# Kernel tuning notes

Measured on AMD Instinct MI355X. Metric: run time of the kernel, lower is better.

## Reference

```python
import jax, jax.numpy as jnp
import numpy as np

B, S, H = 2, 2048, 2048
NH, KVH, HD = 16, 4, 128
R = 16
LORA_SCALE = 32.0 / 16.0  # lora_alpha / lora_r
ATTN_SCALE = HD ** -0.5
NEG = -1e9


def setup_inputs() -> dict:
    key = jax.random.key(0)
    ks = jax.random.split(key, 16)
    q_dim, kv_dim = NH * HD, KVH * HD
    # RoPE tables
    inv_freq = 1.0 / (10000.0 ** (jnp.arange(0, HD, 2, dtype=jnp.float32) / HD))
    ang = jnp.arange(S, dtype=jnp.float32)[:, None] * inv_freq[None, :]  # [S, HD/2]
    emb = jnp.concatenate([ang, ang], axis=-1)  # [S, HD]
    cos = jnp.broadcast_to(jnp.cos(emb)[None], (B, S, HD))
    sin = jnp.broadcast_to(jnp.sin(emb)[None], (B, S, HD))
    # additive causal mask [B,1,S,S]
    causal = jnp.triu(jnp.full((S, S), NEG, dtype=jnp.float32), k=1)
    attention_mask = jnp.broadcast_to(causal[None, None], (B, 1, S, S))
    return {
        'hidden_states': jax.random.normal(ks[0], (B, S, H), jnp.float32),
        'cos': cos,
        'sin': sin,
        'attention_mask': attention_mask,
        'q_w': jax.random.normal(ks[1], (q_dim, H), jnp.float32) * 0.02,
        'k_w': jax.random.normal(ks[2], (kv_dim, H), jnp.float32) * 0.02,
        'v_w': jax.random.normal(ks[3], (kv_dim, H), jnp.float32) * 0.02,
        'q_b': jax.random.normal(ks[4], (q_dim,), jnp.float32) * 0.02,
        'k_b': jax.random.normal(ks[5], (kv_dim,), jnp.float32) * 0.02,
        'v_b': jax.random.normal(ks[6], (kv_dim,), jnp.float32) * 0.02,
        'q_A': jax.random.normal(ks[7], (H, R), jnp.float32) * (1.0 / np.sqrt(H)),
        'q_B': jax.random.normal(ks[8], (R, q_dim), jnp.float32) * 0.02,
        'k_A': jax.random.normal(ks[9], (H, R), jnp.float32) * (1.0 / np.sqrt(H)),
        'k_B': jax.random.normal(ks[10], (R, kv_dim), jnp.float32) * 0.02,
        'v_A': jax.random.normal(ks[11], (H, R), jnp.float32) * (1.0 / np.sqrt(H)),
        'v_B': jax.random.normal(ks[12], (R, kv_dim), jnp.float32) * 0.02,
        'o_w': jax.random.normal(ks[13], (H, H), jnp.float32) * 0.02,
    }


def _rotate_half(x):
    x1, x2 = x[..., : HD // 2], x[..., HD // 2:]
    return jnp.concatenate([-x2, x1], axis=-1)


def reference(hidden_states, cos, sin, attention_mask,
              q_w, k_w, v_w, q_b, k_b, v_b,
              q_A, q_B, k_A, k_B, v_A, v_B, o_w):
    x = hidden_states  # dropout p=0 (eval)
    # fused base + LoRA projections
    q = x @ q_w.T + q_b + LORA_SCALE * ((x @ q_A) @ q_B)  # [B,S,NH*HD]
    k = x @ k_w.T + k_b + LORA_SCALE * ((x @ k_A) @ k_B)  # [B,S,KVH*HD]
    v = x @ v_w.T + v_b + LORA_SCALE * ((x @ v_A) @ v_B)
    q = q.reshape(B, S, NH, HD).transpose(0, 2, 1, 3)   # [B,NH,S,HD]
    k = k.reshape(B, S, KVH, HD).transpose(0, 2, 1, 3)  # [B,KVH,S,HD]
    v = v.reshape(B, S, KVH, HD).transpose(0, 2, 1, 3)
    # RoPE
    c = cos[:, None]  # [B,1,S,HD]
    s = sin[:, None]
    q = q * c + _rotate_half(q) * s
    k = k * c + _rotate_half(k) * s
    # GQA: repeat kv heads
    n_rep = NH // KVH
    k = jnp.repeat(k, n_rep, axis=1)  # [B,NH,S,HD]
    v = jnp.repeat(v, n_rep, axis=1)
    scores = jnp.einsum('bhqd,bhkd->bhqk', q, k) * ATTN_SCALE
    scores = scores + attention_mask
    attn = jax.nn.softmax(scores.astype(jnp.float32), axis=-1).astype(q.dtype)
    out = jnp.einsum('bhqk,bhkd->bhqd', attn, v)
    out = out.transpose(0, 2, 1, 3).reshape(B, S, NH * HD)  # [B,S,H]
    return out @ o_w.T
```

## Files before the change

### kernel.cpp

```cpp
#include <hip/hip_runtime.h>

constexpr int cB   = 2;
constexpr int cS   = 2048;
constexpr int cH   = 2048;
constexpr int cNH  = 16;
constexpr int cKVH = 4;
constexpr int cHD  = 128;
constexpr int cQD  = 2048;
constexpr int cKVD = 512;
constexpr int cNQKV = 3072;
constexpr int cNTOK = 4096;
#define ATTN_SCALE 0.08838834764831845f
#define QSCALE 0.12751589549581288f

typedef __bf16 bf16;
typedef __attribute__((ext_vector_type(8))) __bf16 bf16x8;
typedef __attribute__((ext_vector_type(4))) __bf16 bf16x4;
typedef __attribute__((ext_vector_type(4))) float  f32x4;

__device__ __forceinline__ void async_load16(const bf16* g, bf16* l) {
    __builtin_amdgcn_global_load_lds(
        (const __attribute__((address_space(1))) void*)g,
        (__attribute__((address_space(3))) void*)l, 16, 0, 0);
}

__global__ void conv_f32_bf16(const float* __restrict__ in, bf16* __restrict__ out) {
    int i = (blockIdx.x * 256 + threadIdx.x) * 4;
    f32x4 v = *(const f32x4*)(in + i);
    bf16x4 o;
    o[0] = (bf16)v[0]; o[1] = (bf16)v[1]; o[2] = (bf16)v[2]; o[3] = (bf16)v[3];
    *(bf16x4*)(out + i) = o;
}

__global__ __launch_bounds__(256) void prep_w2(
        const float* __restrict__ qw, const float* __restrict__ kw, const float* __restrict__ vw,
        const float* __restrict__ qA, const float* __restrict__ qB,
        const float* __restrict__ kA, const float* __restrict__ kB,
        const float* __restrict__ vA, const float* __restrict__ vB,
        const float* __restrict__ qb, const float* __restrict__ kbias, const float* __restrict__ vb,
        bf16* __restrict__ Wc, float* __restrict__ biasc) {
    const int wave = threadIdx.x >> 6, lane = threadIdx.x & 63;
    const int n = blockIdx.y * 4 + wave;
    const int k0 = blockIdx.x * 512 + lane * 8;
    const float* W; const float* Am; const float* Bm; const float* bias; int nn, nd;
    if (n < cQD)             { W = qw; Am = qA; Bm = qB; bias = qb;    nn = n;               nd = cQD; }
    else if (n < cQD + cKVD) { W = kw; Am = kA; Bm = kB; bias = kbias; nn = n - cQD;         nd = cKVD; }
    else                     { W = vw; Am = vA; Bm = vB; bias = vb;    nn = n - cQD - cKVD;  nd = cKVD; }
    if (blockIdx.x == 0 && lane == 0) biasc[n] = bias[nn];
    float bm[16];
    #pragma unroll
    for (int r = 0; r < 16; ++r) bm[r] = Bm[r * nd + nn];
    const float* wrow = W + (size_t)nn * cH + k0;
    f32x4 w0 = *(const f32x4*)(wrow);
    f32x4 w1 = *(const f32x4*)(wrow + 4);
    bf16x8 o;
    #pragma unroll
    for (int j = 0; j < 8; ++j) {
        const f32x4* am = (const f32x4*)(Am + (size_t)(k0 + j) * 16);
        f32x4 a0 = am[0], a1 = am[1], a2 = am[2], a3 = am[3];
        float acc = 0.f;
        #pragma unroll
        for (int c = 0; c < 4; ++c) acc += a0[c] * bm[c] + a1[c] * bm[4 + c]
                                         + a2[c] * bm[8 + c] + a3[c] * bm[12 + c];
        const float wv = (j < 4) ? w0[j] : w1[j - 4];
        o[j] = (bf16)(wv + 2.0f * acc);
    }
    *(bf16x8*)&Wc[(size_t)n * cH + k0] = o;
}

__global__ __launch_bounds__(256) void gemm_qkv(const bf16* __restrict__ A, const bf16* __restrict__ Bw,
                                                const float* __restrict__ bias,
                                                const float* __restrict__ cosb, const float* __restrict__ sinb,
                                                bf16* __restrict__ Qr, bf16* __restrict__ Kr,
                                                bf16* __restrict__ Vt) {
    __shared__ bf16 Al[128 * 64];
    __shared__ bf16 Bl[128 * 64];
    const int tid = threadIdx.x;
    const int wave = tid >> 6, lane = tid & 63;
    const int quad = lane >> 4, l16 = lane & 15;
    const int wr = wave >> 1, wc = wave & 1;
    const long bm = (long)blockIdx.y * 128, bn = (long)blockIdx.x * 128;
    const int K = cH;

    f32x4 acc[4][4];
    #pragma unroll
    for (int i = 0; i < 4; ++i)
        #pragma unroll
        for (int c = 0; c < 4; ++c) acc[i][c] = f32x4{0.f, 0.f, 0.f, 0.f};

    int ago[4], slo[4];
    #pragma unroll
    for (int i2 = 0; i2 < 4; ++i2) {
        const int si = i2 * 256 + tid;
        const int row = si >> 3, c8 = si & 7;
        const int csw = c8 ^ (row & 7);
        ago[i2] = row * K + csw * 8;
        slo[i2] = si * 8;
    }
    const size_t bmK = (size_t)bm * K, bnK = (size_t)bn * K;
    const int sw = l16 & 7;

    for (int k0 = 0; k0 < K; k0 += 64) {
        __syncthreads();
        #pragma unroll
        for (int i2 = 0; i2 < 4; ++i2) async_load16(A  + bmK + k0 + ago[i2], Al + slo[i2]);
        #pragma unroll
        for (int i2 = 0; i2 < 4; ++i2) async_load16(Bw + bnK + k0 + ago[i2], Bl + slo[i2]);
        __syncthreads();
        #pragma unroll
        for (int ks = 0; ks < 2; ++ks) {
            const int g = ks * 4 + quad;
            const int cofs = (g ^ sw) * 8;
            bf16x8 af[4], bfr[4];
            #pragma unroll
            for (int i = 0; i < 4; ++i)
                af[i] = *(const bf16x8*)&Al[(wr * 64 + i * 16 + l16) * 64 + cofs];
            #pragma unroll
            for (int c = 0; c < 4; ++c) {
                const int nrow = wc * 32 + (c & 1) * 16 + (c >> 1) * 64 + l16;
                bfr[c] = *(const bf16x8*)&Bl[nrow * 64 + cofs];
            }
            #pragma unroll
            for (int i = 0; i < 4; ++i)
                #pragma unroll
                for (int c = 0; c < 4; ++c)
                    acc[i][c] = __builtin_amdgcn_mfma_f32_16x16x32_bf16(af[i], bfr[c], acc[i][c], 0, 0, 0);
        }
    }

    #pragma unroll
    for (int c = 0; c < 4; ++c) {
        const int nloc = wc * 32 + (c & 1) * 16 + (c >> 1) * 64 + l16;
        const float bv = bias[bn + nloc];
        #pragma unroll
        for (int i = 0; i < 4; ++i)
            #pragma unroll
            for (int r = 0; r < 4; ++r) acc[i][c][r] += bv;
    }

    const int head = (int)(bn >> 7);
    if (head < cNH + cKVH) {
        const bool isQ = head < cNH;
        #pragma unroll
        for (int cl = 0; cl < 2; ++cl) {
            const int d = wc * 32 + cl * 16 + l16;
            #pragma unroll
            for (int i = 0; i < 4; ++i)
                #pragma unroll
                for (int r = 0; r < 4; ++r) {
                    const long t = bm + wr * 64 + i * 16 + quad * 4 + r;
                    const float cv = cosb[t * cHD + d];
                    const float sv = sinb[t * cHD + d];
                    const float v1 = acc[i][cl][r], v2 = acc[i][cl + 2][r];
                    float o1 = v1 * cv - v2 * sv;
                    float o2 = v2 * cv + v1 * sv;
                    if (isQ) { o1 *= QSCALE; o2 *= QSCALE; }
                    const int b = (int)(t >> 11), s = (int)(t & 2047);
                    bf16* dst = isQ
                        ? Qr + ((size_t)(b * cNH + head) * cS + s) * cHD
                        : Kr + ((size_t)(b * cKVH + (head - cNH)) * cS + s) * cHD;
                    dst[d]      = (bf16)o1;
                    dst[d + 64] = (bf16)o2;
                }
        }
    } else {
        const int kv = head - cNH - cKVH;
        const int b = (int)(bm >> 11);
        const int sbase = (int)(bm & 2047);
        #pragma unroll
        for (int c = 0; c < 4; ++c) {
            const int d = wc * 32 + (c & 1) * 16 + (c >> 1) * 64 + l16;
            #pragma unroll
            for (int i = 0; i < 4; ++i) {
                const int s0 = sbase + wr * 64 + i * 16 + quad * 4;
                bf16x4 o4;
                #pragma unroll
                for (int r = 0; r < 4; ++r) o4[r] = (bf16)acc[i][c][r];
                *(bf16x4*)&Vt[((size_t)((b * cKVH + kv) * cHD) + d) * cS + s0] = o4;
            }
        }
    }
}

__global__ __launch_bounds__(256) void gemm_bt_f32(const bf16* __restrict__ A, const bf16* __restrict__ Bw,
                                                   float* __restrict__ Cp, int M, int N, int K) {
    __shared__ bf16 Al[128 * 64];
    __shared__ bf16 Bl[128 * 64];
    const int tid = threadIdx.x;
    const int wave = tid >> 6, lane = tid & 63;
    const int quad = lane >> 4, l16 = lane & 15;
    const int wr = wave >> 1, wc = wave & 1;
    const long bm = (long)blockIdx.y * 128, bn = (long)blockIdx.x * 128;

    f32x4 acc[4][4];
    #pragma unroll
    for (int i = 0; i < 4; ++i)
        #pragma unroll
        for (int c = 0; c < 4; ++c) acc[i][c] = f32x4{0.f, 0.f, 0.f, 0.f};

    int ago[4], slo[4];
    #pragma unroll
    for (int i2 = 0; i2 < 4; ++i2) {
        const int si = i2 * 256 + tid;
        const int row = si >> 3, c8 = si & 7;
        const int csw = c8 ^ (row & 7);
        ago[i2] = row * K + csw * 8;
        slo[i2] = si * 8;
    }
    const size_t bmK = (size_t)bm * K, bnK = (size_t)bn * K;
    const int sw = l16 & 7;

    for (int k0 = 0; k0 < K; k0 += 64) {
        __syncthreads();
        #pragma unroll
        for (int i2 = 0; i2 < 4; ++i2) async_load16(A  + bmK + k0 + ago[i2], Al + slo[i2]);
        #pragma unroll
        for (int i2 = 0; i2 < 4; ++i2) async_load16(Bw + bnK + k0 + ago[i2], Bl + slo[i2]);
        __syncthreads();
        #pragma unroll
        for (int ks = 0; ks < 2; ++ks) {
            const int cofs = ((ks * 4 + quad) ^ sw) * 8;
            bf16x8 af[4], bfr[4];
            #pragma unroll
            for (int i = 0; i < 4; ++i)
                af[i] = *(const bf16x8*)&Al[(wr * 64 + i * 16 + l16) * 64 + cofs];
            #pragma unroll
            for (int c = 0; c < 4; ++c)
                bfr[c] = *(const bf16x8*)&Bl[(wc * 64 + c * 16 + l16) * 64 + cofs];
            #pragma unroll
            for (int i = 0; i < 4; ++i)
                #pragma unroll
                for (int c = 0; c < 4; ++c)
                    acc[i][c] = __builtin_amdgcn_mfma_f32_16x16x32_bf16(af[i], bfr[c], acc[i][c], 0, 0, 0);
        }
    }

    #pragma unroll
    for (int i = 0; i < 4; ++i)
        #pragma unroll
        for (int c = 0; c < 4; ++c) {
            const long m0 = bm + wr * 64 + i * 16 + quad * 4;
            const long n  = bn + wc * 64 + c * 16 + l16;
            #pragma unroll
            for (int r = 0; r < 4; ++r)
                Cp[(m0 + r) * N + n] = acc[i][c][r];
        }
}

__global__ __launch_bounds__(256, 2) void flash4(const bf16* __restrict__ Q, const bf16* __restrict__ K,
                                                 const bf16* __restrict__ Vt, bf16* __restrict__ Ob) {
    __shared__ bf16 kb[8192];
    __shared__ bf16 vb[8192];
    __shared__ bf16 pb[4096];
    const int tid = threadIdx.x;
    const int wave = tid >> 6, lane = tid & 63;
    const int quad = lane >> 4, l16 = lane & 15;
    const int pi = blockIdx.x;
    const int h = blockIdx.y, b = blockIdx.z;

    const bf16* Qh = Q  + (size_t)(b * cNH + h) * cS * cHD;
    const bf16* Kg = K  + (size_t)(b * cKVH + (h >> 2)) * cS * cHD;
    const bf16* Vg = Vt + (size_t)(b * cKVH + (h >> 2)) * cHD * cS;

    int kgo[4], vgo[4], slo[4];
    #pragma unroll
    for (int i2 = 0; i2 < 4; ++i2) {
        const int si = i2 * 256 + tid;
        const int krow = si >> 4, kcsw = si & 15;
        const int kc = (kcsw & 8) | ((kcsw & 7) ^ (krow & 7));
        kgo[i2] = krow * cHD + kc * 8;
        const int vrow = si >> 3, vcsw = si & 7;
        const int vc = vcsw ^ (vrow & 7);
        vgo[i2] = vrow * cS + vc * 8;
        slo[i2] = si * 8;
    }

    #pragma unroll
    for (int t2 = 0; t2 < 2; ++t2) {
        const int qt = t2 == 0 ? (31 - pi) : pi;

        const bf16* Qg = Qh + (size_t)qt * 64 * cHD;
        bf16x8 qf[4];
        #pragma unroll
        for (int ks = 0; ks < 4; ++ks)
            qf[ks] = *(const bf16x8*)(Qg + (size_t)(wave * 16 + l16) * cHD + ks * 32 + quad * 8);

        f32x4 oac[8];
        #pragma unroll
        for (int dt = 0; dt < 8; ++dt) oac[dt] = f32x4{0.f, 0.f, 0.f, 0.f};
        float m_ = -3.0e38f, l_ = 0.f;

        const int nkt = qt + 1;
        for (int kt = 0; kt < nkt; ++kt) {
            __syncthreads();
            const bf16* Kt  = Kg + (size_t)kt * 64 * cHD;
            const bf16* Vtt = Vg + kt * 64;
            #pragma unroll
            for (int i2 = 0; i2 < 4; ++i2) async_load16(Kt + kgo[i2], kb + slo[i2]);
            #pragma unroll
            for (int i2 = 0; i2 < 4; ++i2) async_load16(Vtt + vgo[i2], vb + slo[i2]);
            __syncthreads();

            f32x4 st[4];
            #pragma unroll
            for (int mt = 0; mt < 4; ++mt) {
                bf16x8 kf[4];
                #pragma unroll
                for (int ks = 0; ks < 4; ++ks) {
                    const int c = ks * 4 + quad;
                    const int csw = (c & 8) | ((c & 7) ^ (l16 & 7));
                    kf[ks] = *(const bf16x8*)&kb[(mt * 16 + l16) * 128 + csw * 8];
                }
                f32x4 a = f32x4{0.f, 0.f, 0.f, 0.f};
                #pragma unroll
                for (int ks = 0; ks < 4; ++ks)
                    a = __builtin_amdgcn_mfma_f32_16x16x32_bf16(kf[ks], qf[ks], a, 0, 0, 0);
                st[mt] = a;
            }

            const int qpos = qt * 64 + wave * 16 + l16;
            float tmax = -3.0e38f;
            if ((kt * 64 + 63) > (qt * 64 + wave * 16)) {
                #pragma unroll
                for (int mt = 0; mt < 4; ++mt)
                    #pragma unroll
                    for (int r = 0; r < 4; ++r) {
                        const int kpos = kt * 64 + mt * 16 + quad * 4 + r;
                        if (kpos > qpos) st[mt][r] = -3.0e38f;
                        tmax = fmaxf(tmax, st[mt][r]);
                    }
            } else {
                #pragma unroll
                for (int mt = 0; mt < 4; ++mt)
                    #pragma unroll
                    for (int r = 0; r < 4; ++r) tmax = fmaxf(tmax, st[mt][r]);
            }
            tmax = fmaxf(tmax, __shfl_xor(tmax, 16, 64));
            tmax = fmaxf(tmax, __shfl_xor(tmax, 32, 64));
            const float mnew = fmaxf(m_, tmax);
            if (__any(tmax > m_)) {
                const float alpha = __builtin_amdgcn_exp2f(m_ - mnew);
                l_ *= alpha;
                #pragma unroll
                for (int dt = 0; dt < 8; ++dt)
                    #pragma unroll
                    for (int r = 0; r < 4; ++r) oac[dt][r] *= alpha;
            }
            m_ = mnew;
            float rs = 0.f;
            #pragma unroll
            for (int mt = 0; mt < 4; ++mt)
                #pragma unroll
                for (int r = 0; r < 4; ++r) {
                    const float p = __builtin_amdgcn_exp2f(st[mt][r] - mnew);
                    st[mt][r] = p;
                    rs += p;
                }
            rs += __shfl_xor(rs, 16, 64);
            rs += __shfl_xor(rs, 32, 64);
            l_ += rs;

            #pragma unroll
            for (int mt = 0; mt < 4; ++mt) {
                bf16x4 p4;
                #pragma unroll
                for (int r = 0; r < 4; ++r) p4[r] = (bf16)st[mt][r];
                const int csw = (mt * 2 + (quad >> 1)) ^ (l16 & 7);
                *(bf16x4*)&pb[wave * 1024 + l16 * 64 + csw * 8 + (quad & 1) * 4] = p4;
            }

            bf16x8 pf[2];
            #pragma unroll
            for (int ks = 0; ks < 2; ++ks) {
                const int c = ks * 4 + quad;
                const int csw = c ^ (l16 & 7);
                pf[ks] = *(const bf16x8*)&pb[wave * 1024 + l16 * 64 + csw * 8];
            }
            #pragma unroll
            for (int dt = 0; dt < 8; ++dt) {
                bf16x8 vf[2];
                #pragma unroll
                for (int ks = 0; ks < 2; ++ks) {
                    const int c = ks * 4 + quad;
                    const int csw = c ^ (l16 & 7);
                    vf[ks] = *(const bf16x8*)&vb[(dt * 16 + l16) * 64 + csw * 8];
                }
                #pragma unroll
                for (int ks = 0; ks < 2; ++ks)
                    oac[dt] = __builtin_amdgcn_mfma_f32_16x16x32_bf16(vf[ks], pf[ks], oac[dt], 0, 0, 0);
            }
        }

        const float inv = 1.0f / l_;
        const int token = qt * 64 + wave * 16 + l16;
        bf16* orow = Ob + (size_t)(b * cS + token) * (cNH * cHD) + h * cHD;
        #pragma unroll
        for (int dt = 0; dt < 8; ++dt) {
            bf16x4 o4;
            #pragma unroll
            for (int r = 0; r < 4; ++r) o4[r] = (bf16)(oac[dt][r] * inv);
            *(bf16x4*)&orow[dt * 16 + quad * 4] = o4;
        }
    }
}

extern "C" void kernel_launch(void* const* d_in, const int* in_sizes, int n_in,
                              void* d_out, int out_size, void* d_ws, size_t ws_size,
                              hipStream_t stream) {
    const float* x    = (const float*)d_in[0];
    const float* cosb = (const float*)d_in[1];
    const float* sinb = (const float*)d_in[2];
    const float* qw = (const float*)d_in[4];
    const float* kw = (const float*)d_in[5];
    const float* vw = (const float*)d_in[6];
    const float* qb = (const float*)d_in[7];
    const float* kb_ = (const float*)d_in[8];
    const float* vb = (const float*)d_in[9];
    const float* qA = (const float*)d_in[10];
    const float* qB = (const float*)d_in[11];
    const float* kA = (const float*)d_in[12];
    const float* kB = (const float*)d_in[13];
    const float* vA = (const float*)d_in[14];
    const float* vB = (const float*)d_in[15];
    const float* ow = (const float*)d_in[16];
    float* out = (float*)d_out;

    char* ws = (char*)d_ws;
    bf16* Xbf   = (bf16*)ws;  ws += (size_t)cNTOK * cH * 2;
    bf16* Wc    = (bf16*)ws;  ws += (size_t)cNQKV * cH * 2;
    float* biasc = (float*)ws; ws += (size_t)cNQKV * 4;
    bf16* Qr    = (bf16*)ws;  ws += (size_t)cB * cNH * cS * cHD * 2;
    bf16* Kr    = (bf16*)ws;  ws += (size_t)cB * cKVH * cS * cHD * 2;
    bf16* Vt    = (bf16*)ws;  ws += (size_t)cB * cKVH * cHD * cS * 2;
    bf16* OWbf  = (bf16*)ws;  ws += (size_t)cH * cH * 2;
    bf16* Aout  = (bf16*)ws;  ws += (size_t)cNTOK * cQD * 2;

    conv_f32_bf16<<<(cNTOK * cH) / 1024, 256, 0, stream>>>(x, Xbf);
    conv_f32_bf16<<<(cH * cH) / 1024, 256, 0, stream>>>(ow, OWbf);
    prep_w2<<<dim3(cH / 512, cNQKV / 4), 256, 0, stream>>>(qw, kw, vw, qA, qB, kA, kB, vA, vB,
                                                           qb, kb_, vb, Wc, biasc);

    gemm_qkv<<<dim3(cNQKV / 128, cNTOK / 128), 256, 0, stream>>>(Xbf, Wc, biasc, cosb, sinb, Qr, Kr, Vt);

    flash4<<<dim3(16, cNH, cB), 256, 0, stream>>>(Qr, Kr, Vt, Aout);

    gemm_bt_f32<<<dim3(cH / 128, cNTOK / 128), 256, 0, stream>>>(Aout, OWbf, out, cNTOK, cH, cH);
}
```

Before: 393.8 us.

## Merge prep kernels, deepen GEMM K-tiles, swizzle workgroups, widen flash KV tiles

Folds the two fp32-to-bf16 conversions and the LoRA weight merge into a single launch to save launch overhead. Both GEMMs now load 128-wide K tiles with fewer barriers per K, raise MFMA issue priority, and remap workgroup IDs so neighbouring blocks share operand rows in cache. The flash kernel processes 128-key tiles instead of 64, halving loop iterations and barriers, at the cost of more LDS and registers and coarser causal masking on the diagonal.

```diff
diff --git a/kernel.cpp b/kernel.cpp
--- a/kernel.cpp
+++ b/kernel.cpp
@@ -24,29 +24,42 @@
         (__attribute__((address_space(3))) void*)l, 16, 0, 0);
 }
 
-__global__ void conv_f32_bf16(const float* __restrict__ in, bf16* __restrict__ out) {
-    int i = (blockIdx.x * 256 + threadIdx.x) * 4;
-    f32x4 v = *(const f32x4*)(in + i);
-    bf16x4 o;
-    o[0] = (bf16)v[0]; o[1] = (bf16)v[1]; o[2] = (bf16)v[2]; o[3] = (bf16)v[3];
-    *(bf16x4*)(out + i) = o;
-}
-
-__global__ __launch_bounds__(256) void prep_w2(
+__global__ __launch_bounds__(256) void prep_all(
+        const float* __restrict__ x, bf16* __restrict__ Xbf,
+        const float* __restrict__ ow, bf16* __restrict__ OWbf,
         const float* __restrict__ qw, const float* __restrict__ kw, const float* __restrict__ vw,
         const float* __restrict__ qA, const float* __restrict__ qB,
         const float* __restrict__ kA, const float* __restrict__ kB,
         const float* __restrict__ vA, const float* __restrict__ vB,
         const float* __restrict__ qb, const float* __restrict__ kbias, const float* __restrict__ vb,
         bf16* __restrict__ Wc, float* __restrict__ biasc) {
+    const int bid = blockIdx.x;
+    if (bid < 8192) {
+        const int i = (bid * 256 + threadIdx.x) * 4;
+        f32x4 v = *(const f32x4*)(x + i);
+        bf16x4 o;
+        o[0] = (bf16)v[0]; o[1] = (bf16)v[1]; o[2] = (bf16)v[2]; o[3] = (bf16)v[3];
+        *(bf16x4*)(Xbf + i) = o;
+        return;
+    }
+    if (bid < 12288) {
+        const int i = ((bid - 8192) * 256 + threadIdx.x) * 4;
+        f32x4 v = *(const f32x4*)(ow + i);
+        bf16x4 o;
+        o[0] = (bf16)v[0]; o[1] = (bf16)v[1]; o[2] = (bf16)v[2]; o[3] = (bf16)v[3];
+        *(bf16x4*)(OWbf + i) = o;
+        return;
+    }
+    const int pb = bid - 12288;
+    const int bx = pb & 3, by = pb >> 2;
     const int wave = threadIdx.x >> 6, lane = threadIdx.x & 63;
-    const int n = blockIdx.y * 4 + wave;
-    const int k0 = blockIdx.x * 512 + lane * 8;
+    const int n = by * 4 + wave;
+    const int k0 = bx * 512 + lane * 8;
     const float* W; const float* Am; const float* Bm; const float* bias; int nn, nd;
     if (n < cQD)             { W = qw; Am = qA; Bm = qB; bias = qb;    nn = n;               nd = cQD; }
     else if (n < cQD + cKVD) { W = kw; Am = kA; Bm = kB; bias = kbias; nn = n - cQD;         nd = cKVD; }
     else                     { W = vw; Am = vA; Bm = vB; bias = vb;    nn = n - cQD - cKVD;  nd = cKVD; }
-    if (blockIdx.x == 0 && lane == 0) biasc[n] = bias[nn];
+    if (bx == 0 && lane == 0) biasc[n] = bias[nn];
     float bm[16];
     #pragma unroll
     for (int r = 0; r < 16; ++r) bm[r] = Bm[r * nd + nn];
@@ -68,19 +81,25 @@
     *(bf16x8*)&Wc[(size_t)n * cH + k0] = o;
 }
 
-__global__ __launch_bounds__(256) void gemm_qkv(const bf16* __restrict__ A, const bf16* __restrict__ Bw,
-                                                const float* __restrict__ bias,
-                                                const float* __restrict__ cosb, const float* __restrict__ sinb,
-                                                bf16* __restrict__ Qr, bf16* __restrict__ Kr,
-                                                bf16* __restrict__ Vt) {
-    __shared__ bf16 Al[128 * 64];
-    __shared__ bf16 Bl[128 * 64];
+__global__ __launch_bounds__(256, 2) void gemm_qkv5(const bf16* __restrict__ A, const bf16* __restrict__ Bw,
+                                                    const float* __restrict__ bias,
+                                                    const float* __restrict__ cosb, const float* __restrict__ sinb,
+                                                    bf16* __restrict__ Qr, bf16* __restrict__ Kr,
+                                                    bf16* __restrict__ Vt) {
+    __shared__ bf16 Al[128 * 128];
+    __shared__ bf16 Bl[128 * 128];
     const int tid = threadIdx.x;
     const int wave = tid >> 6, lane = tid & 63;
     const int quad = lane >> 4, l16 = lane & 15;
     const int wr = wave >> 1, wc = wave & 1;
-    const long bm = (long)blockIdx.y * 128, bn = (long)blockIdx.x * 128;
     const int K = cH;
+    constexpr int GX = cNQKV / 128;
+    constexpr int NWG = GX * (cNTOK / 128);
+
+    const int orig = blockIdx.y * GX + blockIdx.x;
+    const int swz = (orig & 7) * (NWG >> 3) + (orig >> 3);
+    const long bm = (long)(swz / GX) * 128;
+    const long bn = (long)(swz % GX) * 128;
 
     f32x4 acc[4][4];
     #pragma unroll
@@ -88,44 +107,59 @@
         #pragma unroll
         for (int c = 0; c < 4; ++c) acc[i][c] = f32x4{0.f, 0.f, 0.f, 0.f};
 
-    int ago[4], slo[4];
-    #pragma unroll
-    for (int i2 = 0; i2 < 4; ++i2) {
+    int ago[8], slo[8];
+    #pragma unroll
+    for (int i2 = 0; i2 < 8; ++i2) {
         const int si = i2 * 256 + tid;
-        const int row = si >> 3, c8 = si & 7;
-        const int csw = c8 ^ (row & 7);
+        const int row = si >> 4, c16 = si & 15;
+        const int csw = (c16 & 8) | ((c16 & 7) ^ (row & 7));
         ago[i2] = row * K + csw * 8;
         slo[i2] = si * 8;
     }
     const size_t bmK = (size_t)bm * K, bnK = (size_t)bn * K;
+
+    auto STAGE = [&](int tt) {
+        const bf16* As_ = A  + bmK + (size_t)tt * 128;
+        const bf16* Bs_ = Bw + bnK + (size_t)tt * 128;
+        #pragma unroll
+        for (int i2 = 0; i2 < 8; ++i2) {
+            async_load16(As_ + ago[i2], &Al[slo[i2]]);
+            async_load16(Bs_ + ago[i2], &Bl[slo[i2]]);
+        }
+    };
+
+    constexpr int NT = cH / 128;
+    STAGE(0);
     const int sw = l16 & 7;
 
-    for (int k0 = 0; k0 < K; k0 += 64) {
-        __syncthreads();
-        #pragma unroll
-        for (int i2 = 0; i2 < 4; ++i2) async_load16(A  + bmK + k0 + ago[i2], Al + slo[i2]);
-        #pragma unroll
-        for (int i2 = 0; i2 < 4; ++i2) async_load16(Bw + bnK + k0 + ago[i2], Bl + slo[i2]);
-        __syncthreads();
-        #pragma unroll
-        for (int ks = 0; ks < 2; ++ks) {
+    for (int t = 0; t < NT; ++t) {
+        asm volatile("s_waitcnt vmcnt(0)" ::: "memory");
+        __builtin_amdgcn_s_barrier();
+        #pragma unroll
+        for (int ks = 0; ks < 4; ++ks) {
             const int g = ks * 4 + quad;
-            const int cofs = (g ^ sw) * 8;
+            const int gsw = (g & 8) | ((g & 7) ^ sw);
+            const int cofs = gsw * 8;
             bf16x8 af[4], bfr[4];
             #pragma unroll
             for (int i = 0; i < 4; ++i)
-                af[i] = *(const bf16x8*)&Al[(wr * 64 + i * 16 + l16) * 64 + cofs];
+                af[i] = *(const bf16x8*)&Al[(wr * 64 + i * 16 + l16) * 128 + cofs];
             #pragma unroll
             for (int c = 0; c < 4; ++c) {
                 const int nrow = wc * 32 + (c & 1) * 16 + (c >> 1) * 64 + l16;
-                bfr[c] = *(const bf16x8*)&Bl[nrow * 64 + cofs];
-            }
+                bfr[c] = *(const bf16x8*)&Bl[nrow * 128 + cofs];
+            }
+            __builtin_amdgcn_s_setprio(1);
             #pragma unroll
             for (int i = 0; i < 4; ++i)
                 #pragma unroll
                 for (int c = 0; c < 4; ++c)
                     acc[i][c] = __builtin_amdgcn_mfma_f32_16x16x32_bf16(af[i], bfr[c], acc[i][c], 0, 0, 0);
-        }
+            __builtin_amdgcn_s_setprio(0);
+        }
+        asm volatile("s_waitcnt lgkmcnt(0)" ::: "memory");
+        __builtin_amdgcn_s_barrier();
+        if (t + 1 < NT) STAGE(t + 1);
     }
 
     #pragma unroll
@@ -182,15 +216,22 @@
     }
 }
 
-__global__ __launch_bounds__(256) void gemm_bt_f32(const bf16* __restrict__ A, const bf16* __restrict__ Bw,
-                                                   float* __restrict__ Cp, int M, int N, int K) {
-    __shared__ bf16 Al[128 * 64];
-    __shared__ bf16 Bl[128 * 64];
+__global__ __launch_bounds__(256, 2) void gemm_oproj5(const bf16* __restrict__ A, const bf16* __restrict__ Bw,
+                                                      float* __restrict__ Cp) {
+    __shared__ bf16 Al[128 * 128];
+    __shared__ bf16 Bl[128 * 128];
     const int tid = threadIdx.x;
     const int wave = tid >> 6, lane = tid & 63;
     const int quad = lane >> 4, l16 = lane & 15;
     const int wr = wave >> 1, wc = wave & 1;
-    const long bm = (long)blockIdx.y * 128, bn = (long)blockIdx.x * 128;
+    constexpr int K = cH, N = cH;
+    constexpr int GX = cH / 128;
+    constexpr int NWG = GX * (cNTOK / 128);
+
+    const int orig = blockIdx.y * GX + blockIdx.x;
+    const int swz = (orig & 7) * (NWG >> 3) + (orig >> 3);
+    const long bm = (long)(swz / GX) * 128;
+    const long bn = (long)(swz % GX) * 128;
 
     f32x4 acc[4][4];
     #pragma unroll
@@ -198,41 +239,57 @@
         #pragma unroll
         for (int c = 0; c < 4; ++c) acc[i][c] = f32x4{0.f, 0.f, 0.f, 0.f};
 
-    int ago[4], slo[4];
-    #pragma unroll
-    for (int i2 = 0; i2 < 4; ++i2) {
+    int ago[8], slo[8];
+    #pragma unroll
+    for (int i2 = 0; i2 < 8; ++i2) {
         const int si = i2 * 256 + tid;
-        const int row = si >> 3, c8 = si & 7;
-        const int csw = c8 ^ (row & 7);
+        const int row = si >> 4, c16 = si & 15;
+        const int csw = (c16 & 8) | ((c16 & 7) ^ (row & 7));
         ago[i2] = row * K + csw * 8;
         slo[i2] = si * 8;
     }
     const size_t bmK = (size_t)bm * K, bnK = (size_t)bn * K;
+
+    auto STAGE = [&](int tt) {
+        const bf16* As_ = A  + bmK + (size_t)tt * 128;
+        const bf16* Bs_ = Bw + bnK + (size_t)tt * 128;
+        #pragma unroll
+        for (int i2 = 0; i2 < 8; ++i2) {
+            async_load16(As_ + ago[i2], &Al[slo[i2]]);
+            async_load16(Bs_ + ago[i2], &Bl[slo[i2]]);
+        }
+    };
+
+    constexpr int NT = K / 128;
+    STAGE(0);
     const int sw = l16 & 7;
 
-    for (int k0 = 0; k0 < K; k0 += 64) {
-        __syncthreads();
-        #pragma unroll
-        for (int i2 = 0; i2 < 4; ++i2) async_load16(A  + bmK + k0 + ago[i2], Al + slo[i2]);
-        #pragma unroll
-        for (int i2 = 0; i2 < 4; ++i2) async_load16(Bw + bnK + k0 + ago[i2], Bl + slo[i2]);
-        __syncthreads();
-        #pragma unroll
-        for (int ks = 0; ks < 2; ++ks) {
-            const int cofs = ((ks * 4 + quad) ^ sw) * 8;
+    for (int t = 0; t < NT; ++t) {
+        asm volatile("s_waitcnt vmcnt(0)" ::: "memory");
+        __builtin_amdgcn_s_barrier();
+        #pragma unroll
+        for (int ks = 0; ks < 4; ++ks) {
+            const int g = ks * 4 + quad;
+            const int gsw = (g & 8) | ((g & 7) ^ sw);
+            const int cofs = gsw * 8;
             bf16x8 af[4], bfr[4];
             #pragma unroll
             for (int i = 0; i < 4; ++i)
-                af[i] = *(const bf16x8*)&Al[(wr * 64 + i * 16 + l16) * 64 + cofs];
+                af[i] = *(const bf16x8*)&Al[(wr * 64 + i * 16 + l16) * 128 + cofs];
             #pragma unroll
             for (int c = 0; c < 4; ++c)
-                bfr[c] = *(const bf16x8*)&Bl[(wc * 64 + c * 16 + l16) * 64 + cofs];
+                bfr[c] = *(const bf16x8*)&Bl[(wc * 64 + c * 16 + l16) * 128 + cofs];
+            __builtin_amdgcn_s_setprio(1);
             #pragma unroll
             for (int i = 0; i < 4; ++i)
                 #pragma unroll
                 for (int c = 0; c < 4; ++c)
                     acc[i][c] = __builtin_amdgcn_mfma_f32_16x16x32_bf16(af[i], bfr[c], acc[i][c], 0, 0, 0);
-        }
+            __builtin_amdgcn_s_setprio(0);
+        }
+        asm volatile("s_waitcnt lgkmcnt(0)" ::: "memory");
+        __builtin_amdgcn_s_barrier();
+        if (t + 1 < NT) STAGE(t + 1);
     }
 
     #pragma unroll
@@ -247,11 +304,11 @@
         }
 }
 
-__global__ __launch_bounds__(256, 2) void flash4(const bf16* __restrict__ Q, const bf16* __restrict__ K,
+__global__ __launch_bounds__(256, 2) void flash6(const bf16* __restrict__ Q, const bf16* __restrict__ K,
                                                  const bf16* __restrict__ Vt, bf16* __restrict__ Ob) {
-    __shared__ bf16 kb[8192];
-    __shared__ bf16 vb[8192];
-    __shared__ bf16 pb[4096];
+    __shared__ bf16 kb[128 * 128];
+    __shared__ bf16 vb[128 * 128];
+    __shared__ bf16 pb[4 * 2048];
     const int tid = threadIdx.x;
     const int wave = tid >> 6, lane = tid & 63;
     const int quad = lane >> 4, l16 = lane & 15;
@@ -262,16 +319,14 @@
     const bf16* Kg = K  + (size_t)(b * cKVH + (h >> 2)) * cS * cHD;
     const bf16* Vg = Vt + (size_t)(b * cKVH + (h >> 2)) * cHD * cS;
 
-    int kgo[4], vgo[4], slo[4];
-    #pragma unroll
-    for (int i2 = 0; i2 < 4; ++i2) {
+    int kgo[8], vgo[8], slo[8];
+    #pragma unroll
+    for (int i2 = 0; i2 < 8; ++i2) {
         const int si = i2 * 256 + tid;
-        const int krow = si >> 4, kcsw = si & 15;
-        const int kc = (kcsw & 8) | ((kcsw & 7) ^ (krow & 7));
-        kgo[i2] = krow * cHD + kc * 8;
-        const int vrow = si >> 3, vcsw = si & 7;
-        const int vc = vcsw ^ (vrow & 7);
-        vgo[i2] = vrow * cS + vc * 8;
+        const int row = si >> 4, c16 = si & 15;
+        const int csw = (c16 & 8) | ((c16 & 7) ^ (row & 7));
+        kgo[i2] = row * cHD + csw * 8;
+        vgo[i2] = row * cS  + csw * 8;
         slo[i2] = si * 8;
     }
 
@@ -290,20 +345,20 @@
         for (int dt = 0; dt < 8; ++dt) oac[dt] = f32x4{0.f, 0.f, 0.f, 0.f};
         float m_ = -3.0e38f, l_ = 0.f;
 
-        const int nkt = qt + 1;
+        const int nkt = (qt >> 1) + 1;
         for (int kt = 0; kt < nkt; ++kt) {
             __syncthreads();
-            const bf16* Kt  = Kg + (size_t)kt * 64 * cHD;
-            const bf16* Vtt = Vg + kt * 64;
-            #pragma unroll
-            for (int i2 = 0; i2 < 4; ++i2) async_load16(Kt + kgo[i2], kb + slo[i2]);
-            #pragma unroll
-            for (int i2 = 0; i2 < 4; ++i2) async_load16(Vtt + vgo[i2], vb + slo[i2]);
+            const bf16* Kt  = Kg + (size_t)kt * 128 * cHD;
+            const bf16* Vtt = Vg + kt * 128;
+            #pragma unroll
+            for (int i2 = 0; i2 < 8; ++i2) async_load16(Kt + kgo[i2], kb + slo[i2]);
+            #pragma unroll
+            for (int i2 = 0; i2 < 8; ++i2) async_load16(Vtt + vgo[i2], vb + slo[i2]);
             __syncthreads();
 
-            f32x4 st[4];
-            #pragma unroll
-            for (int mt = 0; mt < 4; ++mt) {
+            f32x4 st[8];
+            #pragma unroll
+            for (int mt = 0; mt < 8; ++mt) {
                 bf16x8 kf[4];
                 #pragma unroll
                 for (int ks = 0; ks < 4; ++ks) {
@@ -312,26 +367,28 @@
                     kf[ks] = *(const bf16x8*)&kb[(mt * 16 + l16) * 128 + csw * 8];
                 }
                 f32x4 a = f32x4{0.f, 0.f, 0.f, 0.f};
+                __builtin_amdgcn_s_setprio(1);
                 #pragma unroll
                 for (int ks = 0; ks < 4; ++ks)
                     a = __builtin_amdgcn_mfma_f32_16x16x32_bf16(kf[ks], qf[ks], a, 0, 0, 0);
+                __builtin_amdgcn_s_setprio(0);
                 st[mt] = a;
             }
 
             const int qpos = qt * 64 + wave * 16 + l16;
             float tmax = -3.0e38f;
-            if ((kt * 64 + 63) > (qt * 64 + wave * 16)) {
-                #pragma unroll
-                for (int mt = 0; mt < 4; ++mt)
+            if ((kt * 128 + 127) > (qt * 64 + wave * 16)) {
+                #pragma unroll
+                for (int mt = 0; mt < 8; ++mt)
                     #pragma unroll
                     for (int r = 0; r < 4; ++r) {
-                        const int kpos = kt * 64 + mt * 16 + quad * 4 + r;
+                        const int kpos = kt * 128 + mt * 16 + quad * 4 + r;
                         if (kpos > qpos) st[mt][r] = -3.0e38f;
                         tmax = fmaxf(tmax, st[mt][r]);
                     }
             } else {
                 #pragma unroll
-                for (int mt = 0; mt < 4; ++mt)
+                for (int mt = 0; mt < 8; ++mt)
                     #pragma unroll
                     for (int r = 0; r < 4; ++r) tmax = fmaxf(tmax, st[mt][r]);
             }
@@ -349,7 +406,7 @@
             m_ = mnew;
             float rs = 0.f;
             #pragma unroll
-            for (int mt = 0; mt < 4; ++mt)
+            for (int mt = 0; mt < 8; ++mt)
                 #pragma unroll
                 for (int r = 0; r < 4; ++r) {
                     const float p = __builtin_amdgcn_exp2f(st[mt][r] - mnew);
@@ -361,33 +418,36 @@
             l_ += rs;
 
             #pragma unroll
-            for (int mt = 0; mt < 4; ++mt) {
+            for (int mt = 0; mt < 8; ++mt) {
                 bf16x4 p4;
                 #pragma unroll
                 for (int r = 0; r < 4; ++r) p4[r] = (bf16)st[mt][r];
-                const int csw = (mt * 2 + (quad >> 1)) ^ (l16 & 7);
-                *(bf16x4*)&pb[wave * 1024 + l16 * 64 + csw * 8 + (quad & 1) * 4] = p4;
-            }
-
-            bf16x8 pf[2];
-            #pragma unroll
-            for (int ks = 0; ks < 2; ++ks) {
+                const int c16 = mt * 2 + (quad >> 1);
+                const int csw = (c16 & 8) | ((c16 & 7) ^ (l16 & 7));
+                *(bf16x4*)&pb[wave * 2048 + l16 * 128 + csw * 8 + (quad & 1) * 4] = p4;
+            }
+
+            bf16x8 pf[4];
+            #pragma unroll
+            for (int ks = 0; ks < 4; ++ks) {
                 const int c = ks * 4 + quad;
-                const int csw = c ^ (l16 & 7);
-                pf[ks] = *(const bf16x8*)&pb[wave * 1024 + l16 * 64 + csw * 8];
+                const int csw = (c & 8) | ((c & 7) ^ (l16 & 7));
+                pf[ks] = *(const bf16x8*)&pb[wave * 2048 + l16 * 128 + csw * 8];
             }
             #pragma unroll
             for (int dt = 0; dt < 8; ++dt) {
-                bf16x8 vf[2];
-                #pragma unroll
-                for (int ks = 0; ks < 2; ++ks) {
+                bf16x8 vf[4];
+                #pragma unroll
+                for (int ks = 0; ks < 4; ++ks) {
                     const int c = ks * 4 + quad;
-                    const int csw = c ^ (l16 & 7);
-                    vf[ks] = *(const bf16x8*)&vb[(dt * 16 + l16) * 64 + csw * 8];
+                    const int csw = (c & 8) | ((c & 7) ^ (l16 & 7));
+                    vf[ks] = *(const bf16x8*)&vb[(dt * 16 + l16) * 128 + csw * 8];
                 }
-                #pragma unroll
-                for (int ks = 0; ks < 2; ++ks)
+                __builtin_amdgcn_s_setprio(1);
+                #pragma unroll
+                for (int ks = 0; ks < 4; ++ks)
                     oac[dt] = __builtin_amdgcn_mfma_f32_16x16x32_bf16(vf[ks], pf[ks], oac[dt], 0, 0, 0);
+                __builtin_amdgcn_s_setprio(0);
             }
         }
 
@@ -435,14 +495,12 @@
     bf16* OWbf  = (bf16*)ws;  ws += (size_t)cH * cH * 2;
     bf16* Aout  = (bf16*)ws;  ws += (size_t)cNTOK * cQD * 2;
 
-    conv_f32_bf16<<<(cNTOK * cH) / 1024, 256, 0, stream>>>(x, Xbf);
-    conv_f32_bf16<<<(cH * cH) / 1024, 256, 0, stream>>>(ow, OWbf);
-    prep_w2<<<dim3(cH / 512, cNQKV / 4), 256, 0, stream>>>(qw, kw, vw, qA, qB, kA, kB, vA, vB,
-                                                           qb, kb_, vb, Wc, biasc);
-
-    gemm_qkv<<<dim3(cNQKV / 128, cNTOK / 128), 256, 0, stream>>>(Xbf, Wc, biasc, cosb, sinb, Qr, Kr, Vt);
-
-    flash4<<<dim3(16, cNH, cB), 256, 0, stream>>>(Qr, Kr, Vt, Aout);
-
-    gemm_bt_f32<<<dim3(cH / 128, cNTOK / 128), 256, 0, stream>>>(Aout, OWbf, out, cNTOK, cH, cH);
+    prep_all<<<15360, 256, 0, stream>>>(x, Xbf, ow, OWbf, qw, kw, vw, qA, qB, kA, kB, vA, vB,
+                                        qb, kb_, vb, Wc, biasc);
+
+    gemm_qkv5<<<dim3(cNQKV / 128, cNTOK / 128), 256, 0, stream>>>(Xbf, Wc, biasc, cosb, sinb, Qr, Kr, Vt);
+
+    flash6<<<dim3(16, cNH, cB), 256, 0, stream>>>(Qr, Kr, Vt, Aout);
+
+    gemm_oproj5<<<dim3(cH / 128, cNTOK / 128), 256, 0, stream>>>(Aout, OWbf, out);
 }
```

Result: faster. 372.8 us (-5.3%).
